# Performance work log

Hardware: AMD Instinct MI355X
Metric: run time of the kernel (lower is better)

## Reference

```python
import jax, jax.numpy as jnp
import numpy as np

DIM = 768
NUM_HEADS = 12
HEAD_DIM = DIM // NUM_HEADS  # 64
H = W = 48


def setup_inputs() -> dict:
    key = jax.random.key(0)
    ks = jax.random.split(key, 7)
    x = jax.random.normal(ks[0], (2, H, W, DIM), dtype=jnp.float32)
    # qkv Linear: stored as [in, out] for x @ W convention
    qkv_w = jax.random.normal(ks[1], (DIM, 3 * DIM), dtype=jnp.float32) * (DIM ** -0.5)
    qkv_b = jax.random.normal(ks[2], (3 * DIM,), dtype=jnp.float32) * 0.02
    proj_w = jax.random.normal(ks[3], (DIM, DIM), dtype=jnp.float32) * (DIM ** -0.5)
    proj_b = jax.random.normal(ks[4], (DIM,), dtype=jnp.float32) * 0.02
    # decomposed relative position tables (trunc_normal std=0.02 ~ normal*0.02)
    rel_pos_h = jax.random.normal(ks[5], (2 * H - 1, HEAD_DIM), dtype=jnp.float32) * 0.02
    rel_pos_w = jax.random.normal(ks[6], (2 * W - 1, HEAD_DIM), dtype=jnp.float32) * 0.02
    return {"x": x, "qkv_w": qkv_w, "qkv_b": qkv_b, "proj_w": proj_w,
            "proj_b": proj_b, "rel_pos_h": rel_pos_h, "rel_pos_w": rel_pos_w}


def _get_rel_pos(size, rel_pos):
    # q_size == k_size == size; table already has 2*size-1 entries, no interp
    coords = jnp.arange(size)[:, None] - jnp.arange(size)[None, :] + (size - 1)
    return rel_pos[coords]  # [size, size, head_dim]


def reference(x, qkv_w, qkv_b, proj_w, proj_b, rel_pos_h, rel_pos_w):
    B, h, w, dim = x.shape
    nh, hd = NUM_HEADS, HEAD_DIM
    S = h * w
    scale = hd ** -0.5
    qkv = (x.reshape(B, S, dim) @ qkv_w + qkv_b).reshape(B, S, 3, nh, hd)
    qkv = jnp.transpose(qkv, (2, 0, 3, 1, 4)).reshape(3, B * nh, S, hd)
    q, k, v = qkv[0], qkv[1], qkv[2]
    attn = jnp.einsum("bqc,bkc->bqk", q * scale, k)  # [B*nh, S, S]
    # decomposed relative position bias
    Rh = _get_rel_pos(h, rel_pos_h)  # [h, h, hd]
    Rw = _get_rel_pos(w, rel_pos_w)  # [w, w, hd]
    r_q = q.reshape(B * nh, h, w, hd)
    rel_h = jnp.einsum("bhwc,hkc->bhwk", r_q, Rh)  # [B*nh, h, w, h]
    rel_w = jnp.einsum("bhwc,wkc->bhwk", r_q, Rw)  # [B*nh, h, w, w]
    attn = (attn.reshape(B * nh, h, w, h, w)
            + rel_h[:, :, :, :, None]
            + rel_w[:, :, :, None, :]).reshape(B * nh, S, S)
    attn = jax.nn.softmax(attn, axis=-1)
    out = (attn @ v).reshape(B, nh, h, w, hd)
    out = jnp.transpose(out, (0, 2, 3, 1, 4)).reshape(B, h, w, dim)
    return out @ proj_w + proj_b
```

## Files before the change

### kernel.cpp

```cpp
#include <hip/hip_runtime.h>
#include <hip/hip_fp16.h>

#define HD 64
#define SEQ 2304

typedef unsigned short u16;
typedef unsigned int u32;
using f32x4 = __attribute__((ext_vector_type(4))) float;
using s16x8 = __attribute__((ext_vector_type(8))) short;

static __device__ __forceinline__ float bf2f(u16 h) {
  union { float f; u32 u; } a; a.u = ((u32)h) << 16; return a.f;
}
static __device__ __forceinline__ void split2(float x, u16& h, u16& l) {
  u32 u = __float_as_uint(x);
  h = (u16)(u >> 16);
  float r = x - __uint_as_float(u & 0xffff0000u);
  l = (u16)(__float_as_uint(r) >> 16);
}
static __device__ __forceinline__ u16 rne_bf16(float x) {
  u32 u = __float_as_uint(x);
  return (u16)((u + 0x7fffu + ((u >> 16) & 1u)) >> 16);
}

__global__ __launch_bounds__(256) void conv_split_k(
    const float* __restrict__ src, u16* __restrict__ dhi, u16* __restrict__ dlo)
{
  const size_t i = ((size_t)blockIdx.x * 256 + threadIdx.x) * 8;
  f32x4 a = *(const f32x4*)(src + i);
  f32x4 b = *(const f32x4*)(src + i + 4);
  u16 h[8], l[8];
#pragma unroll
  for (int j = 0; j < 8; j++) {
    float x = j < 4 ? a[j] : b[j - 4];
    split2(x, h[j], l[j]);
  }
  *(uint4*)(dhi + i) = *(uint4*)&h[0];
  *(uint4*)(dlo + i) = *(uint4*)&l[0];
}

__global__ __launch_bounds__(256) void conv_wT_k(
    const float* __restrict__ src, u16* __restrict__ dhi, u16* __restrict__ dlo,
    int K, int N)
{
  __shared__ u32 t[64][65];
  const int tid = threadIdx.x;
  const int n0 = blockIdx.x * 64, k0 = blockIdx.y * 64;
  const int r = tid >> 2, c0 = (tid & 3) * 16;
  const float* sp = src + (size_t)(k0 + r) * N + n0 + c0;
#pragma unroll
  for (int j = 0; j < 16; j += 4) {
    f32x4 v = *(const f32x4*)(sp + j);
#pragma unroll
    for (int e = 0; e < 4; e++) {
      u16 h, l;
      split2(v[e], h, l);
      t[r][c0 + j + e] = (u32)h | ((u32)l << 16);
    }
  }
  __syncthreads();
  u16 hb[16], lb[16];
#pragma unroll
  for (int j = 0; j < 16; j++) {
    u32 p = t[c0 + j][r];
    hb[j] = (u16)(p & 0xffffu);
    lb[j] = (u16)(p >> 16);
  }
  size_t off = (size_t)(n0 + r) * K + k0 + c0;
  *(uint4*)(dhi + off)     = *(uint4*)&hb[0];
  *(uint4*)(dhi + off + 8) = *(uint4*)&hb[8];
  *(uint4*)(dlo + off)     = *(uint4*)&lb[0];
  *(uint4*)(dlo + off + 8) = *(uint4*)&lb[8];
}

static __device__ __forceinline__ void load16(
    const u16* pAh, const u16* pAl, const u16* pBh, const u16* pBl, int kk,
    s16x8 ah[4], s16x8 al[4], s16x8 bh[4], s16x8 bl[4])
{
#pragma unroll
  for (int mt = 0; mt < 4; mt++) {
    size_t o = (size_t)mt * 12288 + (size_t)kk * 32;
    ah[mt] = *(const s16x8*)(pAh + o);
    al[mt] = *(const s16x8*)(pAl + o);
    bh[mt] = *(const s16x8*)(pBh + o);
    bl[mt] = *(const s16x8*)(pBl + o);
  }
}
static __device__ __forceinline__ void mfma48(
    const s16x8 ah[4], const s16x8 al[4], const s16x8 bh[4], const s16x8 bl[4],
    f32x4 acc[4][4])
{
#pragma unroll
  for (int mt = 0; mt < 4; mt++)
#pragma unroll
    for (int nt = 0; nt < 4; nt++) {
      acc[mt][nt] = __builtin_amdgcn_mfma_f32_16x16x32_bf16(ah[mt], bh[nt], acc[mt][nt], 0, 0, 0);
      acc[mt][nt] = __builtin_amdgcn_mfma_f32_16x16x32_bf16(ah[mt], bl[nt], acc[mt][nt], 0, 0, 0);
      acc[mt][nt] = __builtin_amdgcn_mfma_f32_16x16x32_bf16(al[mt], bh[nt], acc[mt][nt], 0, 0, 0);
    }
}

__global__ __launch_bounds__(256, 2) void qkv_mfma_k(
    const u16* __restrict__ xhi, const u16* __restrict__ xlo,
    const u16* __restrict__ bthi, const u16* __restrict__ btlo,
    const float* __restrict__ bias,
    float* __restrict__ qbuf, u16* __restrict__ khi, u16* __restrict__ klo,
    u16* __restrict__ vhi)
{
  __shared__ __align__(16) u16 img[4][4096];
  const int tid = threadIdx.x;
  const int lane = tid & 63, wid = tid >> 6;
  const int g = lane >> 4, ql = lane & 15;
  const int wr = wid >> 1, wc = wid & 1;
  const int c0 = blockIdx.x * 128, r0 = blockIdx.y * 128;

  const u16* pAh = xhi  + (size_t)(r0 + wr * 64 + ql) * 768 + g * 8;
  const u16* pAl = xlo  + (size_t)(r0 + wr * 64 + ql) * 768 + g * 8;
  const u16* pBh = bthi + (size_t)(c0 + wc * 64 + ql) * 768 + g * 8;
  const u16* pBl = btlo + (size_t)(c0 + wc * 64 + ql) * 768 + g * 8;

  s16x8 Xah[4], Xal[4], Xbh[4], Xbl[4];
  s16x8 Yah[4], Yal[4], Ybh[4], Ybl[4];
  f32x4 acc[4][4] = {};

  load16(pAh, pAl, pBh, pBl, 0, Xah, Xal, Xbh, Xbl);
  for (int ks = 0; ks < 24; ks += 2) {
    load16(pAh, pAl, pBh, pBl, ks + 1, Yah, Yal, Ybh, Ybl);
    mfma48(Xah, Xal, Xbh, Xbl, acc);
    if (ks + 2 < 24)
      load16(pAh, pAl, pBh, pBl, ks + 2, Xah, Xal, Xbh, Xbl);
    mfma48(Yah, Yal, Ybh, Ybl, acc);
  }

  const int col0 = c0 + wc * 64;
  const int row0 = r0 + wr * 64;
  const int hb36 = col0 >> 6;
  const int which = hb36 / 12, head = hb36 - (hb36 / 12) * 12;
  const int b = row0 / 2304;
  const int sb = row0 - b * 2304;
  const int bh = b * 12 + head;
  float bb[4];
#pragma unroll
  for (int nt = 0; nt < 4; nt++) bb[nt] = bias[col0 + nt * 16 + ql];
#pragma unroll
  for (int mt = 0; mt < 4; mt++)
#pragma unroll
    for (int nt = 0; nt < 4; nt++)
#pragma unroll
      for (int r = 0; r < 4; r++)
        acc[mt][nt][r] += bb[nt];

  if (which == 0) {
#pragma unroll
    for (int mt = 0; mt < 4; mt++)
#pragma unroll
      for (int nt = 0; nt < 4; nt++)
#pragma unroll
        for (int r = 0; r < 4; r++) {
          int s = sb + mt * 16 + g * 4 + r;
          qbuf[((size_t)bh * SEQ + s) * 64 + nt * 16 + ql] = acc[mt][nt][r];
        }
  } else if (which == 1) {
    const int kt = sb >> 6;
    const size_t tile = ((size_t)bh * 36 + kt) * 4096;
    u16* const reg = img[wid];
#pragma unroll
    for (int mt = 0; mt < 4; mt++)
#pragma unroll
      for (int nt = 0; nt < 4; nt++) {
        int pcK = (nt >> 1) * 32 + (ql >> 2) * 8 + (nt & 1) * 4 + (ql & 3);
#pragma unroll
        for (int r = 0; r < 4; r++) {
          u16 h, l;
          split2(acc[mt][nt][r], h, l);
          reg[(mt * 16 + g * 4 + r) * 64 + pcK] = h;
        }
      }
    {
      const u16* src = reg + lane * 64;
      u16* dst = khi + tile + lane * 64;
#pragma unroll
      for (int j = 0; j < 8; j++)
        *(uint4*)(dst + j * 8) = *(const uint4*)(src + j * 8);
    }
#pragma unroll
    for (int mt = 0; mt < 4; mt++)
#pragma unroll
      for (int nt = 0; nt < 4; nt++) {
        int pcK = (nt >> 1) * 32 + (ql >> 2) * 8 + (nt & 1) * 4 + (ql & 3);
#pragma unroll
        for (int r = 0; r < 4; r++) {
          u16 h, l;
          split2(acc[mt][nt][r], h, l);
          reg[(mt * 16 + g * 4 + r) * 64 + pcK] = l;
        }
      }
    {
      const u16* src = reg + lane * 64;
      u16* dst = klo + tile + lane * 64;
#pragma unroll
      for (int j = 0; j < 8; j++)
        *(uint4*)(dst + j * 8) = *(const uint4*)(src + j * 8);
    }
  } else {
    const int kt = sb >> 6;
    const size_t tile = ((size_t)bh * 36 + kt) * 4096;
    u16* const reg = img[wid];
#pragma unroll
    for (int mt = 0; mt < 4; mt++)
#pragma unroll
      for (int nt = 0; nt < 4; nt++)
#pragma unroll
        for (int r = 0; r < 4; r++) {
          int off = (nt * 16 + ql) * 64 + (mt >> 1) * 32 + g * 8 + (mt & 1) * 4 + r;
          reg[off] = rne_bf16(acc[mt][nt][r]);
        }
    {
      const u16* src = reg + lane * 64;
      u16* dst = vhi + tile + lane * 64;
#pragma unroll
      for (int j = 0; j < 8; j++)
        *(uint4*)(dst + j * 8) = *(const uint4*)(src + j * 8);
    }
  }
}

#define BWS_OFF 18432
#define BH_OFF  27648
#define MS_OFF  (BH_OFF + 6372)
#define LS_OFF  (MS_OFF + 256)
__global__ __launch_bounds__(512) void attn_k(
    const float* __restrict__ qb,
    const u16* __restrict__ khi, const u16* __restrict__ klo,
    const u16* __restrict__ vhi,
    const float* __restrict__ rph, const float* __restrict__ rpw,
    u32* __restrict__ aop)
{
  __shared__ __align__(16) char pool[LS_OFF + 256];
  u16* KhiL = (u16*)pool;
  u16* KloL = (u16*)(pool + 9216);
  u16* VhL  = (u16*)(pool + 18432);
  __half* BwS = (__half*)(pool + BWS_OFF);
  __half* Bh  = (__half*)(pool + BH_OFF);
  float* m_s = (float*)(pool + MS_OFF);
  float* l_s = (float*)(pool + LS_OFF);
  float* qlds = (float*)pool;
  float* o_s  = (float*)pool;

  const int tid  = threadIdx.x;
  const int lane = tid & 63;
  const int wid  = tid >> 6;
  const int g    = lane >> 4;
  const int ql   = lane & 15;
  const int wq   = wid & 3;
  const int hh   = wid >> 2;
  const int bh   = blockIdx.x;
  const int qt   = blockIdx.y;
  const int s0   = qt * 64;

  {
    int row = tid >> 3, c0 = (tid & 7) * 8;
    const float* src = qb + ((size_t)bh * SEQ + s0 + row) * HD + c0;
    f32x4 v0 = *(const f32x4*)src;
    f32x4 v1 = *(const f32x4*)(src + 4);
    *(f32x4*)&qlds[row * 68 + c0]     = v0;
    *(f32x4*)&qlds[row * 68 + c0 + 4] = v1;
  }
  __syncthreads();

  s16x8 qfh[2], qfl[2];
  {
    int qrow = wq * 16 + ql;
#pragma unroll
    for (int ds = 0; ds < 2; ds++) {
#pragma unroll
      for (int h2 = 0; h2 < 2; h2++) {
        f32x4 qv = *(const f32x4*)&qlds[qrow * 68 + g * 4 + h2 * 16 + ds * 32];
#pragma unroll
        for (int j = 0; j < 4; j++) {
          u16 hi, lo;
          split2(qv[j], hi, lo);
          qfh[ds][h2 * 4 + j] = (short)hi;
          qfl[ds][h2 * 4 + j] = (short)lo;
        }
      }
    }
  }

  const size_t tbK = (size_t)bh * 36 * 4096;
  const int srow = tid >> 3;
  const int sch  = ((tid & 7) - (srow & 7)) & 7;
  const size_t soff = (size_t)srow * 64 + sch * 8;
  uint4 rkh = *(const uint4*)(khi + tbK + soff);
  uint4 rkl = *(const uint4*)(klo + tbK + soff);
  uint4 rvh = *(const uint4*)(vhi + tbK + soff);

  for (int i = tid; i < 64 * 96; i += 512) {
    int q = i / 96, j = i - (i / 96) * 96;
    int s = s0 + q;
    int qhg = s / 48, qw = s - qhg * 48;
    const float* tab;
    int ridx, col;
    if (j < 48) { col = j;      ridx = qhg - j + 47;        tab = rph; }
    else        { col = j - 48; ridx = qw - (j - 48) + 47;  tab = rpw; }
    const float* rp = tab + (size_t)ridx * HD;
    const float* qp = &qlds[q * 68];
    float s1 = 0.f;
#pragma unroll 4
    for (int d = 0; d < 64; d += 4) {
      f32x4 a = *(const f32x4*)(qp + d);
      f32x4 bv = *(const f32x4*)(rp + d);
      s1 += a[0]*bv[0] + a[1]*bv[1] + a[2]*bv[2] + a[3]*bv[3];
    }
    if (j < 48) Bh[col * 65 + q] = __float2half_rn(s1);
    else        BwS[col * 65 + q] = __float2half_rn(s1);
  }
  __syncthreads();

  const int q64b = wq * 16 + ql;

  float wA[4], wB[4], wC[4];
  {
    float b0[4], b1[4], b2[4];
#pragma unroll
    for (int r = 0; r < 4; r++) {
      b0[r] = __half2float(BwS[(      g * 4 + r) * 65 + q64b]);
      b1[r] = __half2float(BwS[(16 +  g * 4 + r) * 65 + q64b]);
      b2[r] = __half2float(BwS[(32 +  g * 4 + r) * 65 + q64b]);
    }
#pragma unroll
    for (int r = 0; r < 4; r++) {
      wA[r] = hh ? b2[r] : b0[r];
      wB[r] = hh ? b0[r] : b1[r];
      wC[r] = hh ? b1[r] : b2[r];
    }
  }

  float m_r = -3.0e38f, l_r = 0.f;
  f32x4 oacc[4] = {};

#define ATTN_TILE(KT, WA_, WB_, WRAP1) {                                        \
    const int kt = (KT);                                                        \
    __syncthreads();                                                            \
    *(uint4*)(KhiL + srow * 72 + sch * 8) = rkh;                                \
    *(uint4*)(KloL + srow * 72 + sch * 8) = rkl;                                \
    *(uint4*)(VhL  + srow * 72 + sch * 8) = rvh;                                \
    __syncthreads();                                                            \
    if (kt < 35) {                                                              \
      size_t tb = tbK + (size_t)(kt + 1) * 4096;                                \
      rkh = *(const uint4*)(khi + tb + soff);                                   \
      rkl = *(const uint4*)(klo + tb + soff);                                   \
      rvh = *(const uint4*)(vhi + tb + soff);                                   \
    }                                                                           \
    f32x4 sacc[2] = {};                                                         \
    _Pragma("unroll")                                                           \
    for (int ds = 0; ds < 2; ds++) {                                            \
      _Pragma("unroll")                                                         \
      for (int t2 = 0; t2 < 2; t2++) {                                          \
        int row = (hh * 2 + t2) * 16 + ql;                                      \
        s16x8 af = *(const s16x8*)(KhiL + row * 72 + ds * 32 + g * 8);          \
        s16x8 al = *(const s16x8*)(KloL + row * 72 + ds * 32 + g * 8);          \
        sacc[t2] = __builtin_amdgcn_mfma_f32_16x16x32_bf16(af, qfh[ds], sacc[t2], 0, 0, 0); \
        sacc[t2] = __builtin_amdgcn_mfma_f32_16x16x32_bf16(af, qfl[ds], sacc[t2], 0, 0, 0); \
        sacc[t2] = __builtin_amdgcn_mfma_f32_16x16x32_bf16(al, qfh[ds], sacc[t2], 0, 0, 0); \
      }                                                                         \
    }                                                                           \
    u32 kg0 = (u32)(kt * 64 + hh * 32);                                         \
    u32 kh0 = kg0 / 48u;                                                        \
    float bh0v = __half2float(Bh[kh0 * 65 + q64b]);                             \
    float bh1v = __half2float(Bh[(kh0 + 1) * 65 + q64b]);                       \
    float bhB = (WRAP1) ? bh1v : bh0v;                                          \
    float lg[8];                                                                \
    float tmax = -3.0e38f;                                                      \
    _Pragma("unroll")                                                           \
    for (int r = 0; r < 4; r++) {                                               \
      float x0 = sacc[0][r] * 0.125f + (bh0v + WA_[r]);                         \
      float x1 = sacc[1][r] * 0.125f + (bhB  + WB_[r]);                         \
      lg[r]     = x0;                                                           \
      lg[4 + r] = x1;                                                           \
      tmax = fmaxf(tmax, fmaxf(x0, x1));                                        \
    }                                                                           \
    tmax = fmaxf(tmax, __shfl_xor(tmax, 16));                                   \
    tmax = fmaxf(tmax, __shfl_xor(tmax, 32));                                   \
    if (__any(tmax > m_r + 6.0f)) {                                             \
      float mnew = fmaxf(m_r, tmax);                                            \
      float corr = __expf(m_r - mnew);                                          \
      l_r *= corr;                                                              \
      m_r = mnew;                                                               \
      float cq[4];                                                              \
      _Pragma("unroll")                                                         \
      for (int r = 0; r < 4; r++) cq[r] = __shfl(corr, g * 4 + r);              \
      _Pragma("unroll")                                                         \
      for (int dt = 0; dt < 4; dt++)                                            \
        _Pragma("unroll")                                                       \
        for (int r = 0; r < 4; r++) oacc[dt][r] *= cq[r];                       \
    }                                                                           \
    float psum = 0.f;                                                           \
    s16x8 pfh;                                                                  \
    _Pragma("unroll")                                                           \
    for (int j = 0; j < 8; j++) {                                               \
      float p = __expf(lg[j] - m_r);                                            \
      psum += p;                                                                \
      pfh[j] = (short)(u16)(__float_as_uint(p) >> 16);                          \
    }                                                                           \
    psum += __shfl_xor(psum, 16);                                               \
    psum += __shfl_xor(psum, 32);                                               \
    l_r += psum;                                                                \
    _Pragma("unroll")                                                           \
    for (int dt = 0; dt < 4; dt++) {                                            \
      int row = ql + 16 * dt;                                                   \
      s16x8 bhf = *(const s16x8*)(VhL + row * 72 + hh * 32 + g * 8);            \
      oacc[dt] = __builtin_amdgcn_mfma_f32_16x16x32_bf16(pfh, bhf, oacc[dt], 0, 0, 0); \
    }                                                                           \
  }

  for (int kt0 = 0; kt0 < 36; kt0 += 3) {
    ATTN_TILE(kt0 + 0, wA, wB, hh != 0);
    ATTN_TILE(kt0 + 1, wB, wC, false);
    ATTN_TILE(kt0 + 2, wC, wA, hh == 0);
  }
#undef ATTN_TILE

  __syncthreads();
  if (hh == 1) {
    if (g == 0) { m_s[q64b] = m_r; l_s[q64b] = l_r; }
#pragma unroll
    for (int dt = 0; dt < 4; dt++)
#pragma unroll
      for (int r = 0; r < 4; r++)
        o_s[(wq * 16 + g * 4 + r) * 68 + ql + 16 * dt] = oacc[dt][r];
  }
  __syncthreads();
  if (hh == 0) {
    float m2 = m_s[q64b];
    float l2 = l_s[q64b];
    float mf = fmaxf(m_r, m2);
    float c1 = __expf(m_r - mf);
    float c2 = __expf(m2 - mf);
    float lf = l_r * c1 + l2 * c2;
    float c1q[4], c2q[4], lfq[4];
#pragma unroll
    for (int r = 0; r < 4; r++) {
      c1q[r] = __shfl(c1, g * 4 + r);
      c2q[r] = __shfl(c2, g * 4 + r);
      lfq[r] = __shfl(lf, g * 4 + r);
    }
    const int b = bh / 12, head = bh - (bh / 12) * 12;
#pragma unroll
    for (int dt = 0; dt < 4; dt++)
#pragma unroll
      for (int r = 0; r < 4; r++) {
        float oo = oacc[dt][r] * c1q[r]
                 + o_s[(wq * 16 + g * 4 + r) * 68 + ql + 16 * dt] * c2q[r];
        float on = oo / lfq[r];
        int s = s0 + wq * 16 + g * 4 + r;
        size_t idx = ((size_t)b * SEQ + s) * 768 + head * 64 + ql + 16 * dt;
        u16 h, l;
        split2(on, h, l);
        aop[idx] = (u32)h | ((u32)l << 16);
      }
  }
}

__global__ __launch_bounds__(256) void proj_mfma_k(
    const u32* __restrict__ aop,
    const u16* __restrict__ bthi, const u16* __restrict__ btlo,
    const float* __restrict__ bias, float* __restrict__ out)
{
  __shared__ __align__(16) u16 Ah[128*40], Al[128*40], Bh2[128*40], Bl2[128*40];
  const int tid = threadIdx.x;
  const int lane = tid & 63, wid = tid >> 6;
  const int g = lane >> 4, ql = lane & 15;
  const int wr = wid >> 1, wc = wid & 1;
  const int c0 = blockIdx.x * 128, r0 = blockIdx.y * 128;
  const int srow = tid >> 1, half = tid & 1;

  const u32* ag = aop + (size_t)(r0 + srow) * 768 + half * 16;
  const u16* bgh = bthi + (size_t)(c0 + srow) * 768 + half * 16;
  const u16* bgl = btlo + (size_t)(c0 + srow) * 768 + half * 16;

  uint4 paw[4]; uint4 pbh[2], pbl[2];
#pragma unroll
  for (int j = 0; j < 4; j++) paw[j] = *(const uint4*)(ag + j * 4);
  pbh[0] = *(const uint4*)bgh; pbh[1] = *(const uint4*)(bgh + 8);
  pbl[0] = *(const uint4*)bgl; pbl[1] = *(const uint4*)(bgl + 8);

  f32x4 acc[4][4] = {};

  for (int ks = 0; ks < 24; ks++) {
    __syncthreads();
    {
      u16 hb[16], lb[16];
      const u32* pw = (const u32*)&paw[0];
#pragma unroll
      for (int j = 0; j < 16; j++) {
        hb[j] = (u16)(pw[j] & 0xffffu);
        lb[j] = (u16)(pw[j] >> 16);
      }
      u16* d1 = Ah + srow * 40 + half * 16;
      u16* d2 = Al + srow * 40 + half * 16;
      u16* d3 = Bh2 + srow * 40 + half * 16;
      u16* d4 = Bl2 + srow * 40 + half * 16;
      *(uint4*)d1 = *(uint4*)&hb[0]; *(uint4*)(d1 + 8) = *(uint4*)&hb[8];
      *(uint4*)d2 = *(uint4*)&lb[0]; *(uint4*)(d2 + 8) = *(uint4*)&lb[8];
      *(uint4*)d3 = pbh[0]; *(uint4*)(d3 + 8) = pbh[1];
      *(uint4*)d4 = pbl[0]; *(uint4*)(d4 + 8) = pbl[1];
    }
    __syncthreads();
    if (ks < 23) {
      const int o = (ks + 1) * 32;
#pragma unroll
      for (int j = 0; j < 4; j++) paw[j] = *(const uint4*)(ag + o + j * 4);
      pbh[0] = *(const uint4*)(bgh + o); pbh[1] = *(const uint4*)(bgh + o + 8);
      pbl[0] = *(const uint4*)(bgl + o); pbl[1] = *(const uint4*)(bgl + o + 8);
    }
    s16x8 bfh[4], bfl[4];
#pragma unroll
    for (int nt = 0; nt < 4; nt++) {
      bfh[nt] = *(const s16x8*)(Bh2 + (wc * 64 + nt * 16 + ql) * 40 + g * 8);
      bfl[nt] = *(const s16x8*)(Bl2 + (wc * 64 + nt * 16 + ql) * 40 + g * 8);
    }
#pragma unroll
    for (int mt = 0; mt < 4; mt++) {
      s16x8 ah = *(const s16x8*)(Ah + (wr * 64 + mt * 16 + ql) * 40 + g * 8);
      s16x8 al = *(const s16x8*)(Al + (wr * 64 + mt * 16 + ql) * 40 + g * 8);
#pragma unroll
      for (int nt = 0; nt < 4; nt++) {
        acc[mt][nt] = __builtin_amdgcn_mfma_f32_16x16x32_bf16(ah, bfh[nt], acc[mt][nt], 0, 0, 0);
        acc[mt][nt] = __builtin_amdgcn_mfma_f32_16x16x32_bf16(ah, bfl[nt], acc[mt][nt], 0, 0, 0);
        acc[mt][nt] = __builtin_amdgcn_mfma_f32_16x16x32_bf16(al, bfh[nt], acc[mt][nt], 0, 0, 0);
      }
    }
  }
  const int col0 = c0 + wc * 64;
  const int row0 = r0 + wr * 64;
  float bb[4];
#pragma unroll
  for (int nt = 0; nt < 4; nt++) bb[nt] = bias[col0 + nt * 16 + ql];
#pragma unroll
  for (int mt = 0; mt < 4; mt++)
#pragma unroll
    for (int nt = 0; nt < 4; nt++)
#pragma unroll
      for (int r = 0; r < 4; r++)
        out[(size_t)(row0 + mt * 16 + g * 4 + r) * 768 + col0 + nt * 16 + ql] =
            acc[mt][nt][r] + bb[nt];
}

extern "C" void kernel_launch(void* const* d_in, const int* in_sizes, int n_in,
                              void* d_out, int out_size, void* d_ws, size_t ws_size,
                              hipStream_t stream) {
  const float* x      = (const float*)d_in[0];
  const float* qkv_w  = (const float*)d_in[1];
  const float* qkv_b  = (const float*)d_in[2];
  const float* proj_w = (const float*)d_in[3];
  const float* proj_b = (const float*)d_in[4];
  const float* rph    = (const float*)d_in[5];
  const float* rpw    = (const float*)d_in[6];
  float* out = (float*)d_out;
  float* ws  = (float*)d_ws;

  const size_t SZ = (size_t)24 * SEQ * HD;
  float* qbuf = ws;
  u16* khi = (u16*)(ws + SZ);
  u16* klo = khi + SZ;
  u16* vhi = klo + SZ;
  u16* xhi = (u16*)(ws + 3 * SZ);
  u16* xlo = xhi + SZ;
  u32* aop = (u32*)(ws + 4 * SZ);
  u16* wqThi = (u16*)(ws + 5 * SZ);
  u16* wqTlo = wqThi + 768 * 2304;
  u16* wpThi = wqTlo + 768 * 2304;
  u16* wpTlo = wpThi + 768 * 768;

  conv_split_k<<<1728, 256, 0, stream>>>(x, xhi, xlo);
  conv_wT_k <<<dim3(36, 12), 256, 0, stream>>>(qkv_w, wqThi, wqTlo, 768, 2304);
  conv_wT_k <<<dim3(12, 12), 256, 0, stream>>>(proj_w, wpThi, wpTlo, 768, 768);
  qkv_mfma_k<<<dim3(18, 36), 256, 0, stream>>>(xhi, xlo, wqThi, wqTlo, qkv_b,
                                               qbuf, khi, klo, vhi);
  attn_k    <<<dim3(24, 36), 512, 0, stream>>>(qbuf, khi, klo, vhi, rph, rpw, aop);
  proj_mfma_k<<<dim3(6, 36), 256, 0, stream>>>(aop, wpThi, wpTlo, proj_b, out);
}
```

Measured before the change: 456.6 us.

## Load projection GEMM fragments directly from global memory, drop LDS staging

The projection GEMM no longer stages A and B tiles through shared memory with two barriers per k-step. Each wave now loads its MFMA fragments straight from global memory into registers, double-buffered across k-steps, and unpacks the hi/lo bf16 split in registers. This removes the LDS traffic and synchronisation but gives up cross-wave reuse, so each fragment is fetched redundantly by the two waves sharing it, and register pressure rises under launch_bounds(256,2). Separately, the attention kernel moves the cross-lane psum reduction out of the per-tile loop and applies it once to l_r at the end.

```diff
diff --git a/kernel.cpp b/kernel.cpp
--- a/kernel.cpp
+++ b/kernel.cpp
@@ -403,8 +403,6 @@
       psum += p;                                                                \
       pfh[j] = (short)(u16)(__float_as_uint(p) >> 16);                          \
     }                                                                           \
-    psum += __shfl_xor(psum, 16);                                               \
-    psum += __shfl_xor(psum, 32);                                               \
     l_r += psum;                                                                \
     _Pragma("unroll")                                                           \
     for (int dt = 0; dt < 4; dt++) {                                            \
@@ -420,6 +418,9 @@
     ATTN_TILE(kt0 + 2, wC, wA, hh == 0);
   }
 #undef ATTN_TILE
+
+  l_r += __shfl_xor(l_r, 16);
+  l_r += __shfl_xor(l_r, 32);
 
   __syncthreads();
   if (hh == 1) {
@@ -462,76 +463,78 @@
   }
 }
 
-__global__ __launch_bounds__(256) void proj_mfma_k(
+static __device__ __forceinline__ void unpack8(
+    const uint4 w0, const uint4 w1, s16x8& h, s16x8& l)
+{
+  u32 w[8];
+  *(uint4*)&w[0] = w0; *(uint4*)&w[4] = w1;
+  u32 hw[4], lw[4];
+#pragma unroll
+  for (int i = 0; i < 4; i++) {
+    hw[i] = (w[2*i] & 0xffffu) | (w[2*i+1] << 16);
+    lw[i] = (w[2*i] >> 16) | (w[2*i+1] & 0xffff0000u);
+  }
+  h = *(s16x8*)&hw[0];
+  l = *(s16x8*)&lw[0];
+}
+static __device__ __forceinline__ void loadP(
+    const u32* pA, const u16* pBh, const u16* pBl, int kk,
+    uint4 aw[4][2], s16x8 bh[4], s16x8 bl[4])
+{
+#pragma unroll
+  for (int mt = 0; mt < 4; mt++) {
+    size_t oa = (size_t)mt * 12288 + (size_t)kk * 32;
+    aw[mt][0] = *(const uint4*)(pA + oa);
+    aw[mt][1] = *(const uint4*)(pA + oa + 4);
+    size_t ob = (size_t)mt * 12288 + (size_t)kk * 32;
+    bh[mt] = *(const s16x8*)(pBh + ob);
+    bl[mt] = *(const s16x8*)(pBl + ob);
+  }
+}
+static __device__ __forceinline__ void mfmaP(
+    uint4 aw[4][2], const s16x8 bh[4], const s16x8 bl[4], f32x4 acc[4][4])
+{
+#pragma unroll
+  for (int mt = 0; mt < 4; mt++) {
+    s16x8 ah, al;
+    unpack8(aw[mt][0], aw[mt][1], ah, al);
+#pragma unroll
+    for (int nt = 0; nt < 4; nt++) {
+      acc[mt][nt] = __builtin_amdgcn_mfma_f32_16x16x32_bf16(ah, bh[nt], acc[mt][nt], 0, 0, 0);
+      acc[mt][nt] = __builtin_amdgcn_mfma_f32_16x16x32_bf16(ah, bl[nt], acc[mt][nt], 0, 0, 0);
+      acc[mt][nt] = __builtin_amdgcn_mfma_f32_16x16x32_bf16(al, bh[nt], acc[mt][nt], 0, 0, 0);
+    }
+  }
+}
+
+__global__ __launch_bounds__(256, 2) void proj_mfma_k(
     const u32* __restrict__ aop,
     const u16* __restrict__ bthi, const u16* __restrict__ btlo,
     const float* __restrict__ bias, float* __restrict__ out)
 {
-  __shared__ __align__(16) u16 Ah[128*40], Al[128*40], Bh2[128*40], Bl2[128*40];
   const int tid = threadIdx.x;
   const int lane = tid & 63, wid = tid >> 6;
   const int g = lane >> 4, ql = lane & 15;
   const int wr = wid >> 1, wc = wid & 1;
   const int c0 = blockIdx.x * 128, r0 = blockIdx.y * 128;
-  const int srow = tid >> 1, half = tid & 1;
-
-  const u32* ag = aop + (size_t)(r0 + srow) * 768 + half * 16;
-  const u16* bgh = bthi + (size_t)(c0 + srow) * 768 + half * 16;
-  const u16* bgl = btlo + (size_t)(c0 + srow) * 768 + half * 16;
-
-  uint4 paw[4]; uint4 pbh[2], pbl[2];
-#pragma unroll
-  for (int j = 0; j < 4; j++) paw[j] = *(const uint4*)(ag + j * 4);
-  pbh[0] = *(const uint4*)bgh; pbh[1] = *(const uint4*)(bgh + 8);
-  pbl[0] = *(const uint4*)bgl; pbl[1] = *(const uint4*)(bgl + 8);
-
+
+  const u32* pA  = aop  + (size_t)(r0 + wr * 64 + ql) * 768 + g * 8;
+  const u16* pBh = bthi + (size_t)(c0 + wc * 64 + ql) * 768 + g * 8;
+  const u16* pBl = btlo + (size_t)(c0 + wc * 64 + ql) * 768 + g * 8;
+
+  uint4 Xa[4][2]; s16x8 Xbh[4], Xbl[4];
+  uint4 Ya[4][2]; s16x8 Ybh[4], Ybl[4];
   f32x4 acc[4][4] = {};
 
-  for (int ks = 0; ks < 24; ks++) {
-    __syncthreads();
-    {
-      u16 hb[16], lb[16];
-      const u32* pw = (const u32*)&paw[0];
-#pragma unroll
-      for (int j = 0; j < 16; j++) {
-        hb[j] = (u16)(pw[j] & 0xffffu);
-        lb[j] = (u16)(pw[j] >> 16);
-      }
-      u16* d1 = Ah + srow * 40 + half * 16;
-      u16* d2 = Al + srow * 40 + half * 16;
-      u16* d3 = Bh2 + srow * 40 + half * 16;
-      u16* d4 = Bl2 + srow * 40 + half * 16;
-      *(uint4*)d1 = *(uint4*)&hb[0]; *(uint4*)(d1 + 8) = *(uint4*)&hb[8];
-      *(uint4*)d2 = *(uint4*)&lb[0]; *(uint4*)(d2 + 8) = *(uint4*)&lb[8];
-      *(uint4*)d3 = pbh[0]; *(uint4*)(d3 + 8) = pbh[1];
-      *(uint4*)d4 = pbl[0]; *(uint4*)(d4 + 8) = pbl[1];
-    }
-    __syncthreads();
-    if (ks < 23) {
-      const int o = (ks + 1) * 32;
-#pragma unroll
-      for (int j = 0; j < 4; j++) paw[j] = *(const uint4*)(ag + o + j * 4);
-      pbh[0] = *(const uint4*)(bgh + o); pbh[1] = *(const uint4*)(bgh + o + 8);
-      pbl[0] = *(const uint4*)(bgl + o); pbl[1] = *(const uint4*)(bgl + o + 8);
-    }
-    s16x8 bfh[4], bfl[4];
-#pragma unroll
-    for (int nt = 0; nt < 4; nt++) {
-      bfh[nt] = *(const s16x8*)(Bh2 + (wc * 64 + nt * 16 + ql) * 40 + g * 8);
-      bfl[nt] = *(const s16x8*)(Bl2 + (wc * 64 + nt * 16 + ql) * 40 + g * 8);
-    }
-#pragma unroll
-    for (int mt = 0; mt < 4; mt++) {
-      s16x8 ah = *(const s16x8*)(Ah + (wr * 64 + mt * 16 + ql) * 40 + g * 8);
-      s16x8 al = *(const s16x8*)(Al + (wr * 64 + mt * 16 + ql) * 40 + g * 8);
-#pragma unroll
-      for (int nt = 0; nt < 4; nt++) {
-        acc[mt][nt] = __builtin_amdgcn_mfma_f32_16x16x32_bf16(ah, bfh[nt], acc[mt][nt], 0, 0, 0);
-        acc[mt][nt] = __builtin_amdgcn_mfma_f32_16x16x32_bf16(ah, bfl[nt], acc[mt][nt], 0, 0, 0);
-        acc[mt][nt] = __builtin_amdgcn_mfma_f32_16x16x32_bf16(al, bfh[nt], acc[mt][nt], 0, 0, 0);
-      }
-    }
-  }
+  loadP(pA, pBh, pBl, 0, Xa, Xbh, Xbl);
+  for (int ks = 0; ks < 24; ks += 2) {
+    loadP(pA, pBh, pBl, ks + 1, Ya, Ybh, Ybl);
+    mfmaP(Xa, Xbh, Xbl, acc);
+    if (ks + 2 < 24)
+      loadP(pA, pBh, pBl, ks + 2, Xa, Xbh, Xbl);
+    mfmaP(Ya, Ybh, Ybl, acc);
+  }
+
   const int col0 = c0 + wc * 64;
   const int row0 = r0 + wr * 64;
   float bb[4];
```

Measured after the change: 454.2 us. No clear change (-0.5%).
